# Optimization experiments

Measured on AMD Instinct MI355X. Metric: run time of the kernel, lower is better.

## Reference

```python
import jax, jax.numpy as jnp
import numpy as np

T, K, E, H, I = 1024, 2, 8, 2048, 768


def setup_inputs() -> dict:
    key = jax.random.key(0)
    k1, k2, k3, k4, k5 = jax.random.split(key, 5)
    hidden_states = jax.random.normal(k1, (T, H), dtype=jnp.float32)
    top_k_index = jax.random.randint(k2, (T, K), 0, E)
    logits = jax.random.normal(k3, (T, K), dtype=jnp.float32)
    top_k_weights = jax.nn.softmax(logits, axis=-1)  # realistic routing weights
    # Linear-style weights: gate_up [E, 2I, H], down [E, H, I]; scaled like trained params
    gate_up_proj = jax.random.normal(k4, (E, 2 * I, H), dtype=jnp.float32) * 0.02
    down_proj = jax.random.normal(k5, (E, H, I), dtype=jnp.float32) * 0.02
    return {
        "hidden_states": hidden_states,
        "top_k_index": top_k_index,
        "top_k_weights": top_k_weights,
        "gate_up_proj": gate_up_proj,
        "down_proj": down_proj,
    }


def reference(hidden_states, top_k_index, top_k_weights, gate_up_proj, down_proj):
    """Dense-dispatch MoE forward: same math as the per-expert 4-bit loop.

    For every token t and routed expert e (with routing weight w):
      gate, up = split(x_t @ Wgu_e^T); y_t += w * (silu(gate)*up) @ Wd_e^T
    Expressed densely over experts; non-routed (token, expert) pairs get a
    combine weight of 0, so they contribute nothing.
    """
    num_experts = gate_up_proj.shape[0]
    # combine[t, e] = sum_k w[t,k] * [top_k_index[t,k] == e]
    combine = jnp.sum(
        jax.nn.one_hot(top_k_index, num_experts, dtype=hidden_states.dtype)
        * top_k_weights[..., None],
        axis=1,
    )  # [T, E]
    # gate_up: [T, E, 2I]
    gu = jnp.einsum("th,eoh->teo", hidden_states, gate_up_proj)
    gate, up = jnp.split(gu, 2, axis=-1)
    h = jax.nn.silu(gate) * up  # [T, E, I]
    # fold combine weight in before the down projection (scalar per (t,e))
    h = h * combine[:, :, None]
    out = jnp.einsum("tei,ehi->th", h, down_proj)  # [T, H]
    return out.astype(hidden_states.dtype)
```

## Files before the change

### kernel.cpp

```cpp
#include <hip/hip_runtime.h>
#include <hip/hip_bf16.h>

#define T_TOK 1024
#define TOPK  2
#define NEXP  8
#define HDIM  2048
#define IDIM  768
#define MROW  384

typedef __attribute__((ext_vector_type(4))) float f32x4;
typedef __attribute__((ext_vector_type(8))) short bf16x8;
typedef __attribute__((ext_vector_type(8))) unsigned short u16x8;
typedef __attribute__((ext_vector_type(8))) __bf16 bfv8;

__device__ __forceinline__ bf16x8 cvt8(f32x4 v0, f32x4 v1) {
  bfv8 r;
#pragma unroll
  for (int j = 0; j < 4; ++j) { r[j] = (__bf16)v0[j]; r[4 + j] = (__bf16)v1[j]; }
  return __builtin_bit_cast(bf16x8, r);
}

__device__ __forceinline__ void gload_lds16(const void* g, void* l) {
  __builtin_amdgcn_global_load_lds(
      (const __attribute__((address_space(1))) unsigned int*)((unsigned long long)g),
      (__attribute__((address_space(3))) unsigned int*)(unsigned int)(unsigned long long)(l),
      16, 0, 0);
}


__global__ void k_gather(const int* __restrict__ idx, const float* __restrict__ wts,
                         int* __restrict__ cnt, int* __restrict__ tok,
                         float* __restrict__ wl, int* __restrict__ inv) {
  int g = blockIdx.x * 256 + threadIdx.x;
  int e = idx[g];
  float w = wts[g];
  int pos = atomicAdd(&cnt[e], 1);
  if (pos < 2048) { tok[e * 2048 + pos] = g; wl[e * 2048 + pos] = w; }
  inv[g] = (pos < MROW) ? (e * MROW + pos) : -1;
}

__global__ __launch_bounds__(256) void k_compact(const float* __restrict__ x,
                                                 const int* __restrict__ inv,
                                                 unsigned short* __restrict__ xe) {
  int pid = blockIdx.x;
  int iv = inv[pid];
  if (iv < 0) return;
  const float* src = x + (size_t)(pid >> 1) * HDIM;
  unsigned short* dst = xe + (size_t)iv * HDIM;
  int i = threadIdx.x * 8;
  f32x4 a = *(const f32x4*)(src + i);
  f32x4 b = *(const f32x4*)(src + i + 4);
  *(u16x8*)(dst + i) = __builtin_bit_cast(u16x8, cvt8(a, b));
}

__global__ __launch_bounds__(256) void k_gate_up(
    const unsigned short* __restrict__ xe, const float* __restrict__ Wgu,
    const int* __restrict__ cnt, const float* __restrict__ wl,
    unsigned short* __restrict__ hb)
{
  const int b = blockIdx.x;
  const int e = b & 7;
  const int r = b >> 3;
  const int mt = r % 6;
  const int nb = r / 6;
  const int m0 = mt * 64;
  int cc = cnt[e]; if (cc > MROW) cc = MROW;
  if (m0 >= cc) return;
  const int col0 = nb * 32;

  __shared__ unsigned short sA[2][64 * 64];
  __shared__ unsigned short sB[2][64 * 64];
  __shared__ float sW[64];

  const int tid = threadIdx.x;
  const int lane = tid & 63, wid = tid >> 6;

  if (tid < 64) sW[tid] = (m0 + tid < cc) ? wl[e * 2048 + m0 + tid] : 0.f;

  const unsigned short* xeE = xe + ((size_t)e * MROW + m0) * HDIM;
  const unsigned short* aSrc[2];
  unsigned int aDstOff[2];
#pragma unroll
  for (int i = 0; i < 2; ++i) {
    int row = wid * 16 + i * 8 + (lane >> 3);
    int csrc = (lane & 7) ^ (row & 7);
    aSrc[i] = xeE + (size_t)row * HDIM + csrc * 8;
    aDstOff[i] = (unsigned)(wid * 16 + i * 8) * 64;
  }

  const int brow = tid >> 2, cq = (tid & 3);
  const int ocol = (brow < 32) ? (col0 + brow) : (IDIM + col0 + (brow - 32));
  const float* bSrc = Wgu + ((size_t)e * 2 * IDIM + ocol) * HDIM + cq * 16;
  unsigned int bDst[2];
#pragma unroll
  for (int c2 = 0; c2 < 2; ++c2)
    bDst[c2] = (unsigned)(brow * 64 + (((cq * 2 + c2) ^ (brow & 7)) * 8));

  const int fl = lane & 15, q = lane >> 4;
  const int wm = (wid >> 1) * 32, wn = (wid & 1) * 16;

  f32x4 accg[2], accu[2];
#pragma unroll
  for (int mf = 0; mf < 2; ++mf) {
    accg[mf] = f32x4{0.f, 0.f, 0.f, 0.f};
    accu[mf] = f32x4{0.f, 0.f, 0.f, 0.f};
  }

  f32x4 bl[4];

  auto STAGE_ISSUE = [&](int buf, int kt) {
#pragma unroll
    for (int i = 0; i < 2; ++i)
      gload_lds16(aSrc[i] + kt, &sA[buf][aDstOff[i]]);
#pragma unroll
    for (int j = 0; j < 4; ++j)
      bl[j] = *(const f32x4*)(bSrc + kt + j * 4);
  };
  auto STAGE_WRITE = [&](int buf) {
#pragma unroll
    for (int c2 = 0; c2 < 2; ++c2)
      *(bf16x8*)&sB[buf][bDst[c2]] = cvt8(bl[c2 * 2], bl[c2 * 2 + 1]);
  };
  auto COMPUTE = [&](int buf) {
    const unsigned short* A = sA[buf];
    const unsigned short* B = sB[buf];
#pragma unroll
    for (int s = 0; s < 2; ++s) {
      bf16x8 a[2], g2, u2;
#pragma unroll
      for (int mf = 0; mf < 2; ++mf) {
        int rr = wm + mf * 16 + fl;
        a[mf] = *(const bf16x8*)(A + rr * 64 + (((s * 4 + q) ^ (rr & 7)) * 8));
      }
      {
        int rg = wn + fl;
        g2 = *(const bf16x8*)(B + rg * 64 + (((s * 4 + q) ^ (rg & 7)) * 8));
        int ru = 32 + wn + fl;
        u2 = *(const bf16x8*)(B + ru * 64 + (((s * 4 + q) ^ (ru & 7)) * 8));
      }
#pragma unroll
      for (int mf = 0; mf < 2; ++mf) {
        accg[mf] = __builtin_amdgcn_mfma_f32_16x16x32_bf16(a[mf], g2, accg[mf], 0, 0, 0);
        accu[mf] = __builtin_amdgcn_mfma_f32_16x16x32_bf16(a[mf], u2, accu[mf], 0, 0, 0);
      }
    }
  };

  STAGE_ISSUE(0, 0);
  STAGE_WRITE(0);
  __syncthreads();
  int buf = 0;
  for (int kt = 0; kt < HDIM; kt += 64) {
    const int nxt = kt + 64;
    const bool more = nxt < HDIM;
    if (more) STAGE_ISSUE(buf ^ 1, nxt);
    COMPUTE(buf);
    if (more) STAGE_WRITE(buf ^ 1);
    __syncthreads();
    buf ^= 1;
  }

  unsigned short* hbE = hb + (size_t)e * MROW * IDIM;
  const int q4 = q * 4;
#pragma unroll
  for (int mf = 0; mf < 2; ++mf)
#pragma unroll
    for (int v = 0; v < 4; ++v) {
      int rowl = wm + mf * 16 + q4 + v;
      if (m0 + rowl < cc) {
        float g = accg[mf][v], u = accu[mf][v];
        float s = g / (1.f + __expf(-g));
        float h = s * u * sW[rowl];
        hbE[(size_t)(m0 + rowl) * IDIM + col0 + wn + fl] =
            __builtin_bit_cast(unsigned short, (__bf16)h);
      }
    }
}

__global__ __launch_bounds__(256) void k_down(
    const unsigned short* __restrict__ hb, const float* __restrict__ Wd,
    const int* __restrict__ cnt, const int* __restrict__ tok,
    float* __restrict__ out)
{
  const int b = blockIdx.x;
  const int e = b & 7;
  const int r = b >> 3;
  const int mt = r % 6;
  const int nb = r / 6;
  const int m0 = mt * 64;
  int cc = cnt[e]; if (cc > MROW) cc = MROW;
  if (m0 >= cc) return;
  const int col0 = nb * 64;

  __shared__ unsigned short sA[2][64 * 64];
  __shared__ unsigned short sB[2][64 * 64];
  __shared__ int sTok[64];

  const int tid = threadIdx.x;
  const int lane = tid & 63, wid = tid >> 6;
  if (tid < 64) sTok[tid] = (m0 + tid < cc) ? (tok[e * 2048 + m0 + tid] >> 1) : 0;

  const unsigned short* hbE = hb + ((size_t)e * MROW + m0) * IDIM;
  const unsigned short* aSrc[2];
  unsigned int aDstOff[2];
#pragma unroll
  for (int i = 0; i < 2; ++i) {
    int row = wid * 16 + i * 8 + (lane >> 3);
    int csrc = (lane & 7) ^ (row & 7);
    aSrc[i] = hbE + (size_t)row * IDIM + csrc * 8;
    aDstOff[i] = (unsigned)(wid * 16 + i * 8) * 64;
  }

  const int brow = tid >> 2, cq = (tid & 3);
  const float* bSrc = Wd + ((size_t)e * HDIM + col0 + brow) * IDIM + cq * 16;
  unsigned int bDst[2];
#pragma unroll
  for (int c2 = 0; c2 < 2; ++c2)
    bDst[c2] = (unsigned)(brow * 64 + (((cq * 2 + c2) ^ (brow & 7)) * 8));

  const int fl = lane & 15, q = lane >> 4;
  const int wm = (wid >> 1) * 32, wn = (wid & 1) * 32;

  f32x4 acc[2][2];
#pragma unroll
  for (int mf = 0; mf < 2; ++mf)
#pragma unroll
    for (int nf = 0; nf < 2; ++nf) acc[mf][nf] = f32x4{0.f, 0.f, 0.f, 0.f};

  f32x4 bl[4];

  auto STAGE_ISSUE = [&](int buf, int kt) {
#pragma unroll
    for (int i = 0; i < 2; ++i)
      gload_lds16(aSrc[i] + kt, &sA[buf][aDstOff[i]]);
#pragma unroll
    for (int j = 0; j < 4; ++j)
      bl[j] = *(const f32x4*)(bSrc + kt + j * 4);
  };
  auto STAGE_WRITE = [&](int buf) {
#pragma unroll
    for (int c2 = 0; c2 < 2; ++c2)
      *(bf16x8*)&sB[buf][bDst[c2]] = cvt8(bl[c2 * 2], bl[c2 * 2 + 1]);
  };
  auto COMPUTE = [&](int buf) {
    const unsigned short* A = sA[buf];
    const unsigned short* B = sB[buf];
#pragma unroll
    for (int s = 0; s < 2; ++s) {
      bf16x8 a[2], bb[2];
#pragma unroll
      for (int mf = 0; mf < 2; ++mf) {
        int rr = wm + mf * 16 + fl;
        a[mf] = *(const bf16x8*)(A + rr * 64 + (((s * 4 + q) ^ (rr & 7)) * 8));
      }
#pragma unroll
      for (int nf = 0; nf < 2; ++nf) {
        int rn = wn + nf * 16 + fl;
        bb[nf] = *(const bf16x8*)(B + rn * 64 + (((s * 4 + q) ^ (rn & 7)) * 8));
      }
#pragma unroll
      for (int mf = 0; mf < 2; ++mf)
#pragma unroll
        for (int nf = 0; nf < 2; ++nf)
          acc[mf][nf] = __builtin_amdgcn_mfma_f32_16x16x32_bf16(a[mf], bb[nf], acc[mf][nf], 0, 0, 0);
    }
  };

  STAGE_ISSUE(0, 0);
  STAGE_WRITE(0);
  __syncthreads();
  int buf = 0;
  for (int kt = 0; kt < IDIM; kt += 64) {
    const int nxt = kt + 64;
    const bool more = nxt < IDIM;
    if (more) STAGE_ISSUE(buf ^ 1, nxt);
    COMPUTE(buf);
    if (more) STAGE_WRITE(buf ^ 1);
    __syncthreads();
    buf ^= 1;
  }

  const int q4 = q * 4;
#pragma unroll
  for (int mf = 0; mf < 2; ++mf)
#pragma unroll
    for (int nf = 0; nf < 2; ++nf)
#pragma unroll
      for (int v = 0; v < 4; ++v) {
        int rowl = wm + mf * 16 + q4 + v;
        if (m0 + rowl < cc) {
          int t = sTok[rowl];
          atomicAdd(out + (size_t)t * HDIM + col0 + wn + nf * 16 + fl, acc[mf][nf][v]);
        }
      }
}

extern "C" void kernel_launch(void* const* d_in, const int* in_sizes, int n_in,
                              void* d_out, int out_size, void* d_ws, size_t ws_size,
                              hipStream_t stream) {
  const float* x   = (const float*)d_in[0];
  const int*   idx = (const int*)d_in[1];
  const float* wts = (const float*)d_in[2];
  const float* Wgu = (const float*)d_in[3];
  const float* Wd  = (const float*)d_in[4];
  float* out = (float*)d_out;

  char* ws = (char*)d_ws;
  int*            cnt = (int*)(ws + 0);
  int*            tok = (int*)(ws + 64);
  float*          wl  = (float*)(ws + 65600);
  int*            inv = (int*)(ws + 131136);
  unsigned short* xe  = (unsigned short*)(ws + 139328);
  unsigned short* hb  = (unsigned short*)(ws + 12722240);

  hipMemsetAsync(cnt, 0, NEXP * sizeof(int), stream);
  hipMemsetAsync(out, 0, (size_t)T_TOK * HDIM * sizeof(float), stream);
  k_gather<<<dim3((T_TOK * TOPK) / 256), 256, 0, stream>>>(idx, wts, cnt, tok, wl, inv);
  k_compact<<<dim3(T_TOK * TOPK), 256, 0, stream>>>(x, inv, xe);
  k_gate_up<<<dim3(NEXP * 6 * 24), 256, 0, stream>>>(xe, Wgu, cnt, wl, hb);
  k_down<<<dim3(NEXP * 6 * 32), 256, 0, stream>>>(hb, Wd, cnt, tok, out);
}
```

Baseline: 119.8 us.

## Deepen B-operand prefetch to two stages with manual waitcnt and barriers

Restructures the K loops of both grouped GEMM kernels so the fp32 weight tile is prefetched into registers two steps ahead, while the bf16 activation tile goes to LDS one step ahead. Explicit s_waitcnt vmcnt counts and raw s_barrier with sched_barrier replace __syncthreads, so the newest register loads can stay in flight across the barrier. The aim is to hide global-load latency of the weight stream behind MFMA work. It also adds a launch_bounds occupancy hint of 4, which costs more registers for the double register buffers and depends on the vmcnt arithmetic being exact.

Result: no change. 120.2 us (+0.4%).

```diff
diff --git a/kernel.cpp b/kernel.cpp
--- a/kernel.cpp
+++ b/kernel.cpp
@@ -53,7 +53,7 @@
   *(u16x8*)(dst + i) = __builtin_bit_cast(u16x8, cvt8(a, b));
 }
 
-__global__ __launch_bounds__(256) void k_gate_up(
+__global__ __launch_bounds__(256, 4) void k_gate_up(
     const unsigned short* __restrict__ xe, const float* __restrict__ Wgu,
     const int* __restrict__ cnt, const float* __restrict__ wl,
     unsigned short* __restrict__ hb)
@@ -106,21 +106,9 @@
     accu[mf] = f32x4{0.f, 0.f, 0.f, 0.f};
   }
 
-  f32x4 bl[4];
-
-  auto STAGE_ISSUE = [&](int buf, int kt) {
-#pragma unroll
-    for (int i = 0; i < 2; ++i)
-      gload_lds16(aSrc[i] + kt, &sA[buf][aDstOff[i]]);
-#pragma unroll
-    for (int j = 0; j < 4; ++j)
-      bl[j] = *(const f32x4*)(bSrc + kt + j * 4);
-  };
-  auto STAGE_WRITE = [&](int buf) {
-#pragma unroll
-    for (int c2 = 0; c2 < 2; ++c2)
-      *(bf16x8*)&sB[buf][bDst[c2]] = cvt8(bl[c2 * 2], bl[c2 * 2 + 1]);
-  };
+  f32x4 blA[4], blB[4];
+  const int NS = HDIM / 64;
+
   auto COMPUTE = [&](int buf) {
     const unsigned short* A = sA[buf];
     const unsigned short* B = sB[buf];
@@ -146,18 +134,52 @@
     }
   };
 
-  STAGE_ISSUE(0, 0);
-  STAGE_WRITE(0);
-  __syncthreads();
-  int buf = 0;
-  for (int kt = 0; kt < HDIM; kt += 64) {
-    const int nxt = kt + 64;
-    const bool more = nxt < HDIM;
-    if (more) STAGE_ISSUE(buf ^ 1, nxt);
-    COMPUTE(buf);
-    if (more) STAGE_WRITE(buf ^ 1);
-    __syncthreads();
-    buf ^= 1;
+  auto ITER = [&](int ks, f32x4 (&blR)[4], f32x4 (&blW)[4], int bufR) {
+    const int bufW = bufR ^ 1;
+    const bool nA = (ks + 1) < NS;
+    const bool nB = (ks + 2) < NS;
+    if (nA) {
+#pragma unroll
+      for (int i = 0; i < 2; ++i)
+        gload_lds16(aSrc[i] + (ks + 1) * 64, &sA[bufW][aDstOff[i]]);
+    }
+    if (nB) {
+#pragma unroll
+      for (int j = 0; j < 4; ++j)
+        blW[j] = *(const f32x4*)(bSrc + (ks + 2) * 64 + j * 4);
+    }
+    if (nA) {
+#pragma unroll
+      for (int c2 = 0; c2 < 2; ++c2)
+        *(bf16x8*)&sB[bufW][bDst[c2]] = cvt8(blR[c2 * 2], blR[c2 * 2 + 1]);
+    }
+    COMPUTE(bufR);
+    if (nA) {
+      if (nB) { asm volatile("s_waitcnt vmcnt(4) lgkmcnt(0)" ::: "memory"); }
+      else    { asm volatile("s_waitcnt vmcnt(0) lgkmcnt(0)" ::: "memory"); }
+      __builtin_amdgcn_sched_barrier(0);
+      __builtin_amdgcn_s_barrier();
+      __builtin_amdgcn_sched_barrier(0);
+    }
+  };
+
+#pragma unroll
+  for (int j = 0; j < 4; ++j) blA[j] = *(const f32x4*)(bSrc + j * 4);
+#pragma unroll
+  for (int i = 0; i < 2; ++i) gload_lds16(aSrc[i], &sA[0][aDstOff[i]]);
+#pragma unroll
+  for (int j = 0; j < 4; ++j) blB[j] = *(const f32x4*)(bSrc + 64 + j * 4);
+#pragma unroll
+  for (int c2 = 0; c2 < 2; ++c2)
+    *(bf16x8*)&sB[0][bDst[c2]] = cvt8(blA[c2 * 2], blA[c2 * 2 + 1]);
+  asm volatile("s_waitcnt vmcnt(4) lgkmcnt(0)" ::: "memory");
+  __builtin_amdgcn_sched_barrier(0);
+  __builtin_amdgcn_s_barrier();
+  __builtin_amdgcn_sched_barrier(0);
+
+  for (int ks = 0; ks < NS; ks += 2) {
+    ITER(ks,     blB, blA, 0);
+    ITER(ks + 1, blA, blB, 1);
   }
 
   unsigned short* hbE = hb + (size_t)e * MROW * IDIM;
@@ -177,7 +199,7 @@
     }
 }
 
-__global__ __launch_bounds__(256) void k_down(
+__global__ __launch_bounds__(256, 4) void k_down(
     const unsigned short* __restrict__ hb, const float* __restrict__ Wd,
     const int* __restrict__ cnt, const int* __restrict__ tok,
     float* __restrict__ out)
@@ -227,21 +249,9 @@
 #pragma unroll
     for (int nf = 0; nf < 2; ++nf) acc[mf][nf] = f32x4{0.f, 0.f, 0.f, 0.f};
 
-  f32x4 bl[4];
-
-  auto STAGE_ISSUE = [&](int buf, int kt) {
-#pragma unroll
-    for (int i = 0; i < 2; ++i)
-      gload_lds16(aSrc[i] + kt, &sA[buf][aDstOff[i]]);
-#pragma unroll
-    for (int j = 0; j < 4; ++j)
-      bl[j] = *(const f32x4*)(bSrc + kt + j * 4);
-  };
-  auto STAGE_WRITE = [&](int buf) {
-#pragma unroll
-    for (int c2 = 0; c2 < 2; ++c2)
-      *(bf16x8*)&sB[buf][bDst[c2]] = cvt8(bl[c2 * 2], bl[c2 * 2 + 1]);
-  };
+  f32x4 blA[4], blB[4];
+  const int NS = IDIM / 64;
+
   auto COMPUTE = [&](int buf) {
     const unsigned short* A = sA[buf];
     const unsigned short* B = sB[buf];
@@ -266,18 +276,52 @@
     }
   };
 
-  STAGE_ISSUE(0, 0);
-  STAGE_WRITE(0);
-  __syncthreads();
-  int buf = 0;
-  for (int kt = 0; kt < IDIM; kt += 64) {
-    const int nxt = kt + 64;
-    const bool more = nxt < IDIM;
-    if (more) STAGE_ISSUE(buf ^ 1, nxt);
-    COMPUTE(buf);
-    if (more) STAGE_WRITE(buf ^ 1);
-    __syncthreads();
-    buf ^= 1;
+  auto ITER = [&](int ks, f32x4 (&blR)[4], f32x4 (&blW)[4], int bufR) {
+    const int bufW = bufR ^ 1;
+    const bool nA = (ks + 1) < NS;
+    const bool nB = (ks + 2) < NS;
+    if (nA) {
+#pragma unroll
+      for (int i = 0; i < 2; ++i)
+        gload_lds16(aSrc[i] + (ks + 1) * 64, &sA[bufW][aDstOff[i]]);
+    }
+    if (nB) {
+#pragma unroll
+      for (int j = 0; j < 4; ++j)
+        blW[j] = *(const f32x4*)(bSrc + (ks + 2) * 64 + j * 4);
+    }
+    if (nA) {
+#pragma unroll
+      for (int c2 = 0; c2 < 2; ++c2)
+        *(bf16x8*)&sB[bufW][bDst[c2]] = cvt8(blR[c2 * 2], blR[c2 * 2 + 1]);
+    }
+    COMPUTE(bufR);
+    if (nA) {
+      if (nB) { asm volatile("s_waitcnt vmcnt(4) lgkmcnt(0)" ::: "memory"); }
+      else    { asm volatile("s_waitcnt vmcnt(0) lgkmcnt(0)" ::: "memory"); }
+      __builtin_amdgcn_sched_barrier(0);
+      __builtin_amdgcn_s_barrier();
+      __builtin_amdgcn_sched_barrier(0);
+    }
+  };
+
+#pragma unroll
+  for (int j = 0; j < 4; ++j) blA[j] = *(const f32x4*)(bSrc + j * 4);
+#pragma unroll
+  for (int i = 0; i < 2; ++i) gload_lds16(aSrc[i], &sA[0][aDstOff[i]]);
+#pragma unroll
+  for (int j = 0; j < 4; ++j) blB[j] = *(const f32x4*)(bSrc + 64 + j * 4);
+#pragma unroll
+  for (int c2 = 0; c2 < 2; ++c2)
+    *(bf16x8*)&sB[0][bDst[c2]] = cvt8(blA[c2 * 2], blA[c2 * 2 + 1]);
+  asm volatile("s_waitcnt vmcnt(4) lgkmcnt(0)" ::: "memory");
+  __builtin_amdgcn_sched_barrier(0);
+  __builtin_amdgcn_s_barrier();
+  __builtin_amdgcn_sched_barrier(0);
+
+  for (int ks = 0; ks < NS; ks += 2) {
+    ITER(ks,     blB, blA, 0);
+    ITER(ks + 1, blA, blB, 1);
   }
 
   const int q4 = q * 4;
```
